# Kernel optimization log

Hardware: AMD Instinct MI355X
Metric: run time of the kernel (lower is better)

The kernel has to match this reference:

```python
import jax, jax.numpy as jnp
import numpy as np


def setup_inputs() -> dict:
    key = jax.random.key(0)
    k1, k2, k3 = jax.random.split(key, 3)
    B, L, D, E = 32, 4096, 8, 64
    x = jax.random.normal(k1, (B, L, D), dtype=jnp.float32)
    W = jax.random.normal(k2, (D, E), dtype=jnp.float32)
    b = jax.random.normal(k3, (D, E), dtype=jnp.float32)
    return {"x": x, "W": W, "b": b}


def reference(x, W, b):
    # diag_embed(x) @ W + b  ==  x[..., None] * W + b  (elementwise broadcast)
    x_affine = x[..., None] * W + b            # [B, L, D, E]
    # split first embed channel (linear) from the rest (sin-activated)
    x0 = x_affine[..., :1]                     # [B, L, D, 1]
    xr = jnp.sin(x_affine[..., 1:])            # [B, L, D, E-1]
    out = jnp.concatenate([x0, xr], axis=-1)   # [B, L, D, E]
    B, L = x.shape[0], x.shape[1]
    return out.reshape(B, L, -1)               # [B, L, D*E]
```

## Files before the change

kernel.cpp:

```cpp
#include <hip/hip_runtime.h>
#include <math.h>


#define T2V_E   64
#define T2V_DE  512

typedef float fx4 __attribute__((ext_vector_type(4)));

__global__ __launch_bounds__(256) void t2v_kernel(
    const float* __restrict__ x,
    const float* __restrict__ W,
    const float* __restrict__ bias,
    fx4* __restrict__ out)
{
    __shared__ float4 sW[T2V_DE / 4];
    __shared__ float4 sB[T2V_DE / 4];
    const int t = threadIdx.x;
    if (t < T2V_DE / 4) {
        sW[t] = ((const float4*)W)[t];
        sB[t] = ((const float4*)bias)[t];
    }
    __syncthreads();

    const int base = blockIdx.x * 1024 + t;

    const int wi = (base & 127);
    const float4 w = sW[wi];
    const float4 c = sB[wi];

    const int xb = base >> 4;
    float xv[4];
#pragma unroll
    for (int k = 0; k < 4; ++k) xv[k] = x[xb + k * 16];

#pragma unroll
    for (int k = 0; k < 4; ++k) {
        const int i = base + k * 256;
        float ax = fmaf(xv[k], w.x, c.x);
        float ay = fmaf(xv[k], w.y, c.y);
        float az = fmaf(xv[k], w.z, c.z);
        float aw = fmaf(xv[k], w.w, c.w);
        fx4 o;
        o.x = ((i & 15) == 0) ? ax : __sinf(ax);
        o.y = __sinf(ay);
        o.z = __sinf(az);
        o.w = __sinf(aw);
        out[i] = o;
    }
}

extern "C" void kernel_launch(void* const* d_in, const int* in_sizes, int n_in,
                              void* d_out, int out_size, void* d_ws, size_t ws_size,
                              hipStream_t stream) {
    const float* x    = (const float*)d_in[0];
    const float* W    = (const float*)d_in[1];
    const float* bias = (const float*)d_in[2];
    fx4* out = (fx4*)d_out;

    const int blocks = (out_size >> 2) / 1024;
    t2v_kernel<<<blocks, 256, 0, stream>>>(x, W, bias, out);
}
```

Measured before the change: 267.3 us.

## Use fixed-size persistent grid with per-thread loop and drop shared-memory staging

Replaces the launch of one block per 1024 float4 outputs with a fixed grid of 2048 blocks. Each thread loops over a contiguous chunk in steps of 8 unrolled iterations, and W and bias are loaded straight into registers once per thread instead of being staged in shared memory behind a barrier. This cuts block launch and sync overhead and gives more independent stores in flight per thread. The cost is fewer waves for latency hiding, and the code assumes the output size divides evenly by the block and iteration counts.

```diff
diff --git a/kernel.cpp b/kernel.cpp
--- a/kernel.cpp
+++ b/kernel.cpp
@@ -2,8 +2,9 @@
 #include <math.h>
 
 
-#define T2V_E   64
-#define T2V_DE  512
+#define NTHR   256
+#define NBLK   2048
+#define UNROLL 8
 
 typedef float fx4 __attribute__((ext_vector_type(4)));
 
@@ -11,41 +12,41 @@
     const float* __restrict__ x,
     const float* __restrict__ W,
     const float* __restrict__ bias,
-    fx4* __restrict__ out)
+    fx4* __restrict__ out,
+    int total_f4)
 {
-    __shared__ float4 sW[T2V_DE / 4];
-    __shared__ float4 sB[T2V_DE / 4];
-    const int t = threadIdx.x;
-    if (t < T2V_DE / 4) {
-        sW[t] = ((const float4*)W)[t];
-        sB[t] = ((const float4*)bias)[t];
-    }
-    __syncthreads();
+    const int t  = threadIdx.x;
+    const int wi = t & 127;
+    const float4 w = ((const float4*)W)[wi];
+    const float4 c = ((const float4*)bias)[wi];
+    const bool  e0 = (wi & 15) == 0;
 
-    const int base = blockIdx.x * 1024 + t;
+    const int per_block = total_f4 / NBLK;
+    const int iters     = per_block / NTHR;
+    const int base      = blockIdx.x * per_block + t;
+    const int xbase     = (blockIdx.x * per_block) >> 4;
+    const int xt        = t >> 4;
 
-    const int wi = (base & 127);
-    const float4 w = sW[wi];
-    const float4 c = sB[wi];
-
-    const int xb = base >> 4;
-    float xv[4];
+    for (int it0 = 0; it0 < iters; it0 += UNROLL) {
+        float xv[UNROLL];
 #pragma unroll
-    for (int k = 0; k < 4; ++k) xv[k] = x[xb + k * 16];
+        for (int u = 0; u < UNROLL; ++u)
+            xv[u] = x[xbase + (it0 + u) * 16 + xt];
 
 #pragma unroll
-    for (int k = 0; k < 4; ++k) {
-        const int i = base + k * 256;
-        float ax = fmaf(xv[k], w.x, c.x);
-        float ay = fmaf(xv[k], w.y, c.y);
-        float az = fmaf(xv[k], w.z, c.z);
-        float aw = fmaf(xv[k], w.w, c.w);
-        fx4 o;
-        o.x = ((i & 15) == 0) ? ax : __sinf(ax);
-        o.y = __sinf(ay);
-        o.z = __sinf(az);
-        o.w = __sinf(aw);
-        out[i] = o;
+        for (int u = 0; u < UNROLL; ++u) {
+            const int i = base + (it0 + u) * 256;
+            float ax = fmaf(xv[u], w.x, c.x);
+            float ay = fmaf(xv[u], w.y, c.y);
+            float az = fmaf(xv[u], w.z, c.z);
+            float aw = fmaf(xv[u], w.w, c.w);
+            fx4 o;
+            o.x = e0 ? ax : __sinf(ax);
+            o.y = __sinf(ay);
+            o.z = __sinf(az);
+            o.w = __sinf(aw);
+            out[i] = o;
+        }
     }
 }
 
@@ -57,6 +58,6 @@
     const float* bias = (const float*)d_in[2];
     fx4* out = (fx4*)d_out;
 
-    const int blocks = (out_size >> 2) / 1024;
-    t2v_kernel<<<blocks, 256, 0, stream>>>(x, W, bias, out);
+    const int total_f4 = out_size >> 2;
+    t2v_kernel<<<NBLK, NTHR, 0, stream>>>(x, W, bias, out, total_f4);
 }
```

Result: no change. 265.0 us (-0.9%).
